# Kernel tuning notes

Hardware: AMD Instinct MI355X
Metric: run time of the kernel (lower is better)

The kernel has to match this reference:

```python
import jax, jax.numpy as jnp
import numpy as np

NEG_SLOPE = 0.2
K_L = 0.5
K_G = 0.5
TEMP_G = 1e-3


def _leaky(v):
    return jnp.where(v >= 0, v, NEG_SLOPE * v)


def _topk_row_mask(scores, keep):
    # scores: [n, n, h]; torch.topk(dim=0) -> indices [keep, n] per head,
    # then head_mask[indices, :] = 1 selects whole ROWS (any column hit).
    n = scores.shape[0]
    s = jnp.transpose(scores, (1, 2, 0))        # [n_cols, h, n_rows]
    _, idx = jax.lax.top_k(s, keep)             # [n_cols, h, keep]

    def per_head(idx_h):                        # idx_h: [n_cols, keep]
        return jnp.zeros((n,), scores.dtype).at[idx_h.reshape(-1)].set(1.0)

    rows = jax.vmap(per_head, in_axes=1, out_axes=0)(idx)  # [h, n_rows]
    return jnp.transpose(rows)[:, None, :]      # [n_rows, 1, h] broadcast over cols


def setup_inputs() -> dict:
    key = jax.random.key(0)
    ks = jax.random.split(key, 8)
    n, in_f, feat_dim = 1024, 256, 128
    H, F = 4, 64                                # n_heads, n_hidden (out_features=256)
    feats = jax.random.normal(ks[0], (n, feat_dim), dtype=jnp.float32)
    x = jax.random.normal(ks[1], (n, in_f), dtype=jnp.float32)
    adj = jax.random.randint(ks[2], (n, n, 1), 0, 2).astype(jnp.int32)
    sc = 0.05
    W_l = jax.random.normal(ks[3], (in_f, H * F), dtype=jnp.float32) * sc
    W_r = jax.random.normal(ks[4], (in_f, H * F), dtype=jnp.float32) * sc
    attn_w = jax.random.normal(ks[5], (F,), dtype=jnp.float32) * sc
    W_delta = jax.random.normal(ks[6], (2 * F, F), dtype=jnp.float32) * sc
    b_delta = jnp.zeros((F,), dtype=jnp.float32)
    return {"feats": feats, "x": x, "adj": adj, "W_l": W_l, "W_r": W_r,
            "attn_w": attn_w, "W_delta": W_delta, "b_delta": b_delta}


def reference(feats, x, adj, W_l, W_r, attn_w, W_delta, b_delta):
    n = x.shape[0]
    F = attn_w.shape[0]
    H = W_l.shape[1] // F
    g_l = (x @ W_l).reshape(n, H, F)
    g_r = (x @ W_r).reshape(n, H, F)
    # g_sum[i, j] = g_l[j] + g_r[i]  (repeat vs repeat_interleave ordering)
    g_sum = g_r[:, None, :, :] + g_l[None, :, :, :]          # [n, n, H, F]
    e = jnp.einsum('ijhf,f->ijh', _leaky(g_sum), attn_w)     # [n, n, H]

    mask_adj = adj > 0                                        # [n, n, 1]
    a_l = jax.nn.softmax(jnp.where(mask_adj, e, -jnp.inf), axis=1)
    a_1nd = a_l * mask_adj.astype(e.dtype)

    keep_l = int(n * (1.0 - K_L))
    a_filt = a_1nd * _topk_row_mask(a_1nd, keep_l)
    attn_local = jnp.einsum('ijh,jhf->ihf', a_filt, g_r)     # [n, H, F]

    omega = jax.nn.softmax(e, axis=1)
    fn = (feats - feats.min(axis=0)) / (feats.max(axis=0) - feats.min(axis=0))
    fn = jnp.where(jnp.isnan(fn), 0.0, fn)
    g_rn = (g_r - g_r.min(axis=0)) / (g_r.max(axis=0) - g_r.min(axis=0))
    nf = jnp.linalg.norm(fn, axis=1)                          # [n] (index j)
    ng = jnp.linalg.norm(g_rn, axis=2)                        # [n, H] (index i)
    alpha = jax.nn.softmax(jnp.abs(nf[None, :, None] - ng[:, None, :]), axis=1)
    gamma = 0.5 * (omega + (1.0 - alpha))

    keep_g = int(n * (1.0 - K_G))
    gf = gamma * _topk_row_mask(gamma, keep_g)
    gf = jax.nn.softmax(jnp.where(gf == 0, 1e-10, gf) / TEMP_G, axis=1)
    attn_global = jnp.einsum('ijh,jhf->ihf', gf, g_r)         # [n, H, F]

    inter = _leaky(jnp.concatenate([attn_local, attn_global], axis=2) @ W_delta + b_delta)
    delta = jax.nn.softmax(inter, axis=1)                     # softmax over heads (torch dim=1)
    attn_res = delta * attn_local + (1.0 - delta) * attn_global
    return attn_res.reshape(n, H * F)
```

## Files before the change

### kernel.cpp

```cpp
#include <hip/hip_runtime.h>
#include <cstdint>
#include <cstddef>

#define N 1024
#define HN 4
#define FDIM 64
#define KSEL 512
#define FLT_MAX_ 3.402823466e+38f

__device__ __forceinline__ float wred_sum(float v){
#pragma unroll
  for(int o=32;o>0;o>>=1) v += __shfl_down(v,o,64);
  return v;
}
__device__ __forceinline__ float bfly_sum(float v){
#pragma unroll
  for(int o=1;o<64;o<<=1) v += __shfl_xor(v,o,64);
  return v;
}
__device__ __forceinline__ float bfly_max(float v){
#pragma unroll
  for(int o=1;o<64;o<<=1) v = fmaxf(v,__shfl_xor(v,o,64));
  return v;
}
__device__ __forceinline__ int bfly_sumi(int v){
#pragma unroll
  for(int o=1;o<64;o<<=1) v += __shfl_xor(v,o,64);
  return v;
}
__device__ __forceinline__ float bred_sum(float v, float* scr){
  int t=threadIdx.x;
  v = wred_sum(v);
  __syncthreads();
  if((t&63)==0) scr[t>>6]=v;
  __syncthreads();
  return (scr[0]+scr[1])+(scr[2]+scr[3]);
}

__global__ __launch_bounds__(256) void stage1(const float* __restrict__ x,
                                              const float* __restrict__ W_l,
                                              const float* __restrict__ W_r,
                                              const int* __restrict__ adj,
                                              const float* __restrict__ feats,
                                              float* __restrict__ g_l,
                                              float* __restrict__ g_r,
                                              unsigned* __restrict__ adjbit,
                                              int* __restrict__ masks,
                                              float* __restrict__ pmin_f,
                                              float* __restrict__ pmax_f){
  int bx = blockIdx.x, t = threadIdx.x;
  if(bx < 512){
    const float* __restrict__ W = (bx >= 256) ? W_r : W_l;
    float* __restrict__ g = (bx >= 256) ? g_r : g_l;
    int i0 = (bx & 255)*4;
    float acc[4] = {0.f,0.f,0.f,0.f};
#pragma unroll 8
    for(int k=0;k<256;k++){
      float w = W[(size_t)k*256 + t];
#pragma unroll
      for(int r=0;r<4;r++) acc[r] = fmaf(x[(size_t)(i0+r)*256 + k], w, acc[r]);
    }
#pragma unroll
    for(int r=0;r<4;r++) g[(size_t)(i0+r)*256 + t] = acc[r];
  } else if(bx < 1536){
    int i = bx - 512, w = t>>6, lane = t&63;
    if(i < 32) masks[i*256 + t] = 0;
#pragma unroll
    for(int it=0; it<4; it++){
      int j = w*256 + it*64 + lane;
      int v = adj[(size_t)i*N + j];
      unsigned long long mb = __ballot(v > 0);
      if(lane == 0){
        adjbit[i*32 + w*8 + it*2]     = (unsigned)mb;
        adjbit[i*32 + w*8 + it*2 + 1] = (unsigned)(mb >> 32);
      }
    }
  } else {
    int chunk = bx - 1536;
    if(t < 128){
      float lo = FLT_MAX_, hi = -FLT_MAX_;
      int r0 = chunk*64;
      for(int r=0;r<64;r++){
        float v = feats[(size_t)(r0+r)*128 + t];
        lo = fminf(lo,v); hi = fmaxf(hi,v);
      }
      pmin_f[chunk*128+t]=lo; pmax_f[chunk*128+t]=hi;
    }
  }
}

__global__ __launch_bounds__(256) void stage2(const float* __restrict__ g_l,
                                              const float* __restrict__ g_r,
                                              const float* __restrict__ attn_w,
                                              const float* __restrict__ feats,
                                              const float* __restrict__ pmin_f, const float* __restrict__ pmax_f,
                                              float* __restrict__ pmin_g, float* __restrict__ pmax_g,
                                              float* __restrict__ nf,
                                              float* __restrict__ e,
                                              float* __restrict__ eT){
  __shared__ __align__(16) float smem[2*64*68 + 128];
  int bx = blockIdx.x, t = threadIdx.x;
  if(bx < 1024){
    float* grs = smem;
    float* gls = smem + 64*68;
    float* aw  = smem + 2*64*68;
    float* aw2 = aw + 64;
    int h = bx >> 8, i0 = ((bx>>4)&15)*64, j0 = (bx&15)*64;
    if(t < 64){ float w = attn_w[t]; aw[t]=w; aw2[t]=0.2f*w; }
#pragma unroll
    for(int k=0;k<16;k++){
      int idx = t + k*256; int r = idx>>6, f = idx&63;
      grs[r*68+f] = g_r[(size_t)(i0+r)*256 + h*64 + f];
      gls[r*68+f] = g_l[(size_t)(j0+r)*256 + h*64 + f];
    }
    __syncthreads();
    int tj = t&15, ti = t>>4;
    float acc[4][4];
#pragma unroll
    for(int a=0;a<4;a++)
#pragma unroll
      for(int b=0;b<4;b++) acc[a][b]=0.f;
    for(int fc=0; fc<64; fc+=4){
      float4 wv  = *(float4*)&aw[fc];
      float4 wv2 = *(float4*)&aw2[fc];
      float4 ga4[4], gb4[4];
#pragma unroll
      for(int a=0;a<4;a++) ga4[a] = *(float4*)&grs[(ti*4+a)*68+fc];
#pragma unroll
      for(int b=0;b<4;b++) gb4[b] = *(float4*)&gls[(tj+16*b)*68+fc];
#pragma unroll
      for(int a=0;a<4;a++)
#pragma unroll
        for(int b=0;b<4;b++){
          float s0 = ga4[a].x + gb4[b].x;
          float s1 = ga4[a].y + gb4[b].y;
          float s2 = ga4[a].z + gb4[b].z;
          float s3 = ga4[a].w + gb4[b].w;
          acc[a][b] = fmaf(s0, (s0>=0.f)?wv.x:wv2.x, acc[a][b]);
          acc[a][b] = fmaf(s1, (s1>=0.f)?wv.y:wv2.y, acc[a][b]);
          acc[a][b] = fmaf(s2, (s2>=0.f)?wv.z:wv2.z, acc[a][b]);
          acc[a][b] = fmaf(s3, (s3>=0.f)?wv.w:wv2.w, acc[a][b]);
        }
    }
#pragma unroll
    for(int a=0;a<4;a++)
#pragma unroll
      for(int b=0;b<4;b++){
        int i = i0 + ti*4 + a, j = j0 + tj + 16*b;
        e[((size_t)h*N + i)*N + j] = acc[a][b];
      }
    __syncthreads();
    float* esT = smem;
#pragma unroll
    for(int a=0;a<4;a++)
#pragma unroll
      for(int b=0;b<4;b++)
        esT[(tj + 16*b)*68 + ti*4 + a] = acc[a][b];
    __syncthreads();
#pragma unroll
    for(int k=0;k<4;k++){
      int jl = (t>>4) + 16*k, ilx = (t&15)*4;
      *(float4*)(eT + ((size_t)h*N + j0 + jl)*N + i0 + ilx) = *(float4*)&esT[jl*68 + ilx];
    }
  } else if(bx < 1040){
    int chunk = bx - 1024;
    float lo = FLT_MAX_, hi = -FLT_MAX_;
    int r0 = chunk*64;
    for(int r=0;r<64;r++){
      float v = g_r[(size_t)(r0+r)*256 + t];
      lo = fminf(lo,v); hi = fmaxf(hi,v);
    }
    pmin_g[chunk*256+t]=lo; pmax_g[chunk*256+t]=hi;
  } else {
    int i = bx - 1040;
    float* scr = smem;
    float u = 0.f;
    if(t < 128){
      float lo = FLT_MAX_, hi = -FLT_MAX_;
#pragma unroll
      for(int k=0;k<16;k++){
        lo = fminf(lo, pmin_f[k*128+t]);
        hi = fmaxf(hi, pmax_f[k*128+t]);
      }
      float d = hi - lo;
      float v = feats[(size_t)i*128 + t];
      u = (d==0.f) ? 0.f : (v - lo)/d;
    }
    float tot = bred_sum(u*u, scr);
    if(t==0) nf[i] = sqrtf(tot);
  }
}

__global__ __launch_bounds__(256) void row_stats(const float* __restrict__ e,
                                                 const unsigned* __restrict__ adjbit,
                                                 const float* __restrict__ nf,
                                                 const float* __restrict__ g_r,
                                                 const float* __restrict__ pmin_g, const float* __restrict__ pmax_g,
                                                 float* __restrict__ ng,
                                                 float* __restrict__ mlA, float* __restrict__ islA,
                                                 float* __restrict__ moA, float* __restrict__ isoA,
                                                 float* __restrict__ maA, float* __restrict__ isaA,
                                                 float* __restrict__ mgA, float* __restrict__ sgA){
  int i = blockIdx.x, t = threadIdx.x, h = t>>6, lane = t&63;
  float glo = FLT_MAX_, ghi = -FLT_MAX_;
#pragma unroll
  for(int k=0;k<16;k++){
    glo = fminf(glo, pmin_g[k*256 + h*64 + lane]);
    ghi = fmaxf(ghi, pmax_g[k*256 + h*64 + lane]);
  }
  float dg = ghi - glo;
  float ug = (g_r[(size_t)i*256 + h*64 + lane] - glo)/dg;
  float ngv = sqrtf(bfly_sum(ug*ug));
  if(lane==0) ng[h*N + i] = ngv;

  size_t base = ((size_t)h*N + i)*N;
  float er[16], nfr[16];
  unsigned nib[4];
#pragma unroll
  for(int c=0;c<4;c++){
    float4 e4 = *(const float4*)(e  + base + c*256 + lane*4);
    float4 n4 = *(const float4*)(nf + c*256 + lane*4);
    er[c*4+0]=e4.x; er[c*4+1]=e4.y; er[c*4+2]=e4.z; er[c*4+3]=e4.w;
    nfr[c*4+0]=n4.x; nfr[c*4+1]=n4.y; nfr[c*4+2]=n4.z; nfr[c*4+3]=n4.w;
    nib[c] = (adjbit[i*32 + c*8 + (lane>>3)] >> ((lane&7)*4)) & 0xFu;
  }
  float ml=-FLT_MAX_, mo=-FLT_MAX_, ma=-FLT_MAX_;
#pragma unroll
  for(int c=0;c<4;c++)
#pragma unroll
    for(int k=0;k<4;k++){
      int q = c*4+k;
      float ev = er[q];
      mo = fmaxf(mo, ev);
      if((nib[c]>>k)&1) ml = fmaxf(ml, ev);
      ma = fmaxf(ma, fabsf(nfr[q]-ngv));
    }
  ml = bfly_max(ml); mo = bfly_max(mo); ma = bfly_max(ma);
  float sl=0.f, so=0.f, sa=0.f;
#pragma unroll
  for(int c=0;c<4;c++)
#pragma unroll
    for(int k=0;k<4;k++){
      int q = c*4+k;
      float ev = er[q];
      so += __expf(ev-mo);
      if((nib[c]>>k)&1) sl += __expf(ev-ml);
      sa += __expf(fabsf(nfr[q]-ngv)-ma);
    }
  sl = bfly_sum(sl); so = bfly_sum(so); sa = bfly_sum(sa);
  float isl = 1.f/sl, iso = 1.f/so, isa = 1.f/sa;
  float gg[16];
  float mg = -FLT_MAX_;
#pragma unroll
  for(int q=0;q<16;q++){
    float ev = er[q];
    float omega = __expf(ev-mo)*iso;
    float alpha = __expf(fabsf(nfr[q]-ngv)-ma)*isa;
    float g = 0.5f*(omega + 1.f - alpha);
    gg[q] = g;
    mg = fmaxf(mg, g);
  }
  mg = bfly_max(mg);
  float sg = 0.f;
#pragma unroll
  for(int q=0;q<16;q++) sg += __expf((gg[q]-mg)/1e-3f);
  sg = bfly_sum(sg);
  if(lane==0){
    mlA[h*N+i]=ml; islA[h*N+i]=isl;
    moA[h*N+i]=mo; isoA[h*N+i]=iso;
    maA[h*N+i]=ma; isaA[h*N+i]=isa;
    mgA[h*N+i]=mg; sgA[h*N+i]=sg;
  }
}

__device__ __forceinline__ void apply_mask(const unsigned* ur, unsigned T, int tneed, int EQ,
                                           int* __restrict__ mask, int base, int lane){
  if(EQ == tneed){
#pragma unroll
    for(int c=0;c<4;c++)
#pragma unroll
      for(int k2=0;k2<4;k2++){
        int i = c*256 + lane*4 + k2;
        if(ur[c*4+k2] >= T) mask[base + i] = 1;
      }
  } else {
    int run_base = 0;
#pragma unroll
    for(int c=0;c<4;c++){
      int tc=0;
      unsigned long long bm[4];
#pragma unroll
      for(int k2=0;k2<4;k2++){
        bm[k2] = __ballot(ur[c*4+k2]==T);
        tc += (ur[c*4+k2]==T)?1:0;
      }
      unsigned long long lower = (lane==0) ? 0ull : (~0ull >> (64-lane));
      int run = run_base;
#pragma unroll
      for(int k2=0;k2<4;k2++) run += (int)__popcll(bm[k2] & lower);
#pragma unroll
      for(int k2=0;k2<4;k2++){
        int i = c*256 + lane*4 + k2;
        unsigned u = ur[c*4+k2];
        bool sel = (u > T) || (u == T && run < tneed);
        run += (u==T)?1:0;
        if(sel) mask[base + i] = 1;
      }
      int ctot = 0;
#pragma unroll
      for(int k2=0;k2<4;k2++) ctot += (int)__popcll(bm[k2]);
      run_base += ctot;
    }
  }
}

__global__ __launch_bounds__(256) void colselect9(const float* __restrict__ eT,
                                                  const unsigned* __restrict__ adjbit,
                                                  const float* __restrict__ nf,
                                                  const float* __restrict__ mlA, const float* __restrict__ islA,
                                                  const float* __restrict__ moA, const float* __restrict__ isoA,
                                                  const float* __restrict__ maA, const float* __restrict__ isaA,
                                                  const float* __restrict__ ngA,
                                                  int* __restrict__ mask_l,
                                                  int* __restrict__ mask_g){
  int t = threadIdx.x, w = t>>6, lane = t&63;
  int gcol = blockIdx.x*4 + w;
  int z  = gcol >> 12;
  int hj = gcol & 4095;
  int h  = hj >> 10, jc = hj & 1023;
  const float* __restrict__ src = eT + (size_t)hj * (size_t)N;

  float ev[16];
#pragma unroll
  for(int c=0;c<4;c++){
    float4 e4 = ((const float4*)src)[c*64 + lane];
    ev[c*4+0]=e4.x; ev[c*4+1]=e4.y; ev[c*4+2]=e4.z; ev[c*4+3]=e4.w;
  }
  unsigned ur[16];
  if(z == 0){
    int wo = jc >> 5; unsigned bm = 1u << (jc & 31);
#pragma unroll
    for(int c=0;c<4;c++){
      int ib = (h<<10) + c*256 + lane*4;
      float4 ml4 = *(const float4*)(mlA+ib);
      float4 il4 = *(const float4*)(islA+ib);
      float mlv[4] = {ml4.x,ml4.y,ml4.z,ml4.w};
      float ilv[4] = {il4.x,il4.y,il4.z,il4.w};
#pragma unroll
      for(int k=0;k<4;k++){
        int i = c*256 + lane*4 + k;
        float a = (adjbit[i*32 + wo] & bm) ? __expf(ev[c*4+k]-mlv[k])*ilv[k] : 0.f;
        ur[c*4+k] = __float_as_uint(a);
      }
    }
  } else {
    float nfv = nf[jc];
#pragma unroll
    for(int c=0;c<4;c++){
      int ib = (h<<10) + c*256 + lane*4;
      float4 mo4 = *(const float4*)(moA+ib);
      float4 io4 = *(const float4*)(isoA+ib);
      float4 ma4 = *(const float4*)(maA+ib);
      float4 ia4 = *(const float4*)(isaA+ib);
      float4 ng4 = *(const float4*)(ngA+ib);
      float mov[4]={mo4.x,mo4.y,mo4.z,mo4.w}, iov[4]={io4.x,io4.y,io4.z,io4.w};
      float mav[4]={ma4.x,ma4.y,ma4.z,ma4.w}, iav[4]={ia4.x,ia4.y,ia4.z,ia4.w};
      float ngv[4]={ng4.x,ng4.y,ng4.z,ng4.w};
#pragma unroll
      for(int k=0;k<4;k++){
        float omega = __expf(ev[c*4+k]-mov[k])*iov[k];
        float alpha = __expf(fabsf(nfv-ngv[k])-mav[k])*iav[k];
        float g = 0.5f*(omega + 1.f - alpha);
        ur[c*4+k] = __float_as_uint(g);
      }
    }
  }

  unsigned prefix = 0u;
  for(int b=30; b>=0; b--){
    unsigned cand = prefix | (1u<<b);
    int c = 0;
#pragma unroll
    for(int q=0;q<16;q++) c += (int)__popcll(__ballot(ur[q] >= cand));
    prefix = (c >= KSEL) ? cand : prefix;
  }
  unsigned T = prefix;
  int GT = 0, EQ = 0;
#pragma unroll
  for(int q=0;q<16;q++){
    GT += (int)__popcll(__ballot(ur[q] > T));
    EQ += (int)__popcll(__ballot(ur[q] == T));
  }
  int tneed = KSEL - GT;

  int* __restrict__ mask = z ? mask_g : mask_l;
  apply_mask(ur, T, tneed, EQ, mask, h<<10, lane);
}

__global__ __launch_bounds__(256) void attn_mm2(const float* __restrict__ eT,
                                                const float* __restrict__ g_r,
                                                const unsigned* __restrict__ adjbit,
                                                const float* __restrict__ nf,
                                                const float* __restrict__ mlA, const float* __restrict__ islA,
                                                const float* __restrict__ moA, const float* __restrict__ isoA,
                                                const float* __restrict__ maA, const float* __restrict__ isaA,
                                                const float* __restrict__ ngA,
                                                const float* __restrict__ mgA, const float* __restrict__ sgA,
                                                const int* __restrict__ mask_g,
                                                float* __restrict__ partL,
                                                float* __restrict__ partG){
  __shared__ __align__(16) float a_t[2][32][36];
  __shared__ __align__(16) float p_t[2][32][36];
  __shared__ __align__(16) float b_s[2][32][68];
  int i0 = blockIdx.x*32, h = blockIdx.y, s = blockIdx.z, j0 = s*128;
  int t = threadIdx.x;
  int il = t & 31, jq = t >> 5;
  int gi = h*N + i0 + il;
  float ml_r = mlA[gi], il_r = islA[gi];
  float mo_r = moA[gi], io_r = isoA[gi];
  float ma_r = maA[gi], ia_r = isaA[gi];
  float ng_r = ngA[gi];
  float mg_r = mgA[gi], isg_r = 1.f/sgA[gi];
  int   mgf_r = mask_g[gi];
  int fq = t & 15, iq = t >> 4;
  int jb2a = t>>4, d4a = t&15;
  int idxb = t + 256, jb2b = idxb>>4, d4b = idxb&15;

  float e0,e1,e2,e3; unsigned aw; float4 nf4, vb0, vb1;
  {
    int jb = j0;
    size_t ebase = ((size_t)h*N + jb + jq*4)*(size_t)N + i0 + il;
    e0 = eT[ebase]; e1 = eT[ebase+N]; e2 = eT[ebase+2*N]; e3 = eT[ebase+3*N];
    aw = adjbit[(size_t)(i0+il)*32 + s*4 + 0];
    nf4 = *(const float4*)(nf + jb + jq*4);
    vb0 = *(const float4*)(g_r + (size_t)(jb+jb2a)*256 + h*64 + d4a*4);
    vb1 = *(const float4*)(g_r + (size_t)(jb+jb2b)*256 + h*64 + d4b*4);
  }
  {
    const float inv = 1.f/1024.f;
    float evs[4] = {e0,e1,e2,e3};
    float nfsv[4] = {nf4.x,nf4.y,nf4.z,nf4.w};
#pragma unroll
    for(int c=0;c<4;c++){
      int jl = jq*4 + c;
      float a = ((aw >> jl) & 1u) ? __expf(evs[c]-ml_r)*il_r : 0.f;
      float omega = __expf(evs[c]-mo_r)*io_r;
      float alpha = __expf(fabsf(nfsv[c]-ng_r)-ma_r)*ia_r;
      float g = 0.5f*(omega + 1.f - alpha);
      float p = mgf_r ? __expf((g-mg_r)/1e-3f)*isg_r : inv;
      a_t[0][jl][il] = a;
      p_t[0][jl][il] = p;
    }
    *(float4*)&b_s[0][jb2a][d4a*4] = vb0;
    *(float4*)&b_s[0][jb2b][d4b*4] = vb1;
  }
  float4 accL[2], accG[2];
#pragma unroll
  for(int r=0;r<2;r++){ accL[r]=make_float4(0,0,0,0); accG[r]=make_float4(0,0,0,0); }

  for(int sub=0; sub<4; sub++){
    int cur = sub & 1;
    __syncthreads();
    if(sub < 3){
      int jb = j0 + (sub+1)*32;
      size_t ebase = ((size_t)h*N + jb + jq*4)*(size_t)N + i0 + il;
      e0 = eT[ebase]; e1 = eT[ebase+N]; e2 = eT[ebase+2*N]; e3 = eT[ebase+3*N];
      aw = adjbit[(size_t)(i0+il)*32 + s*4 + sub + 1];
      nf4 = *(const float4*)(nf + jb + jq*4);
      vb0 = *(const float4*)(g_r + (size_t)(jb+jb2a)*256 + h*64 + d4a*4);
      vb1 = *(const float4*)(g_r + (size_t)(jb+jb2b)*256 + h*64 + d4b*4);
    }
#pragma unroll 8
    for(int j=0;j<32;j++){
      float4 bv = *(float4*)&b_s[cur][j][fq*4];
      float2 av = *(float2*)&a_t[cur][j][iq*2];
      float2 pv = *(float2*)&p_t[cur][j][iq*2];
      accL[0].x = fmaf(av.x, bv.x, accL[0].x); accL[0].y = fmaf(av.x, bv.y, accL[0].y);
      accL[0].z = fmaf(av.x, bv.z, accL[0].z); accL[0].w = fmaf(av.x, bv.w, accL[0].w);
      accL[1].x = fmaf(av.y, bv.x, accL[1].x); accL[1].y = fmaf(av.y, bv.y, accL[1].y);
      accL[1].z = fmaf(av.y, bv.z, accL[1].z); accL[1].w = fmaf(av.y, bv.w, accL[1].w);
      accG[0].x = fmaf(pv.x, bv.x, accG[0].x); accG[0].y = fmaf(pv.x, bv.y, accG[0].y);
      accG[0].z = fmaf(pv.x, bv.z, accG[0].z); accG[0].w = fmaf(pv.x, bv.w, accG[0].w);
      accG[1].x = fmaf(pv.y, bv.x, accG[1].x); accG[1].y = fmaf(pv.y, bv.y, accG[1].y);
      accG[1].z = fmaf(pv.y, bv.z, accG[1].z); accG[1].w = fmaf(pv.y, bv.w, accG[1].w);
    }
    if(sub < 3){
      int nxt = 1 - cur;
      const float inv = 1.f/1024.f;
      float evs[4] = {e0,e1,e2,e3};
      float nfsv[4] = {nf4.x,nf4.y,nf4.z,nf4.w};
#pragma unroll
      for(int c=0;c<4;c++){
        int jl = jq*4 + c;
        float a = ((aw >> jl) & 1u) ? __expf(evs[c]-ml_r)*il_r : 0.f;
        float omega = __expf(evs[c]-mo_r)*io_r;
        float alpha = __expf(fabsf(nfsv[c]-ng_r)-ma_r)*ia_r;
        float g = 0.5f*(omega + 1.f - alpha);
        float p = mgf_r ? __expf((g-mg_r)/1e-3f)*isg_r : inv;
        a_t[nxt][jl][il] = a;
        p_t[nxt][jl][il] = p;
      }
      *(float4*)&b_s[nxt][jb2a][d4a*4] = vb0;
      *(float4*)&b_s[nxt][jb2b][d4b*4] = vb1;
    }
  }
#pragma unroll
  for(int r=0;r<2;r++){
    int i = i0 + iq*2 + r;
    size_t o = ((size_t)s*N + i)*256 + h*64 + fq*4;
    *(float4*)&partL[o] = accL[r];
    *(float4*)&partG[o] = accG[r];
  }
}

__global__ __launch_bounds__(256) void epilogue(const float* __restrict__ partL,
                                                const float* __restrict__ partG,
                                                const int* __restrict__ mask_l,
                                                const float* __restrict__ W_delta,
                                                const float* __restrict__ b_delta,
                                                float* __restrict__ out){
  __shared__ float cat[4][128];
  __shared__ float inter_s[4][64];
  int i = blockIdx.x, t = threadIdx.x;
  int h = t>>6, f = t&63;
  float sl = 0.f, sg = 0.f;
#pragma unroll
  for(int s2=0;s2<8;s2++){
    size_t o = ((size_t)s2*N + i)*256 + h*64 + f;
    sl += partL[o];
    sg += partG[o];
  }
  if(!mask_l[h*N + i]) sl = 0.f;
  cat[h][f]      = sl;
  cat[h][64 + f] = sg;
  __syncthreads();
  float d = b_delta[f];
  for(int c=0;c<128;c++) d = fmaf(cat[h][c], W_delta[(size_t)c*64 + f], d);
  d = (d >= 0.f) ? d : 0.2f*d;
  inter_s[h][f] = d;
  __syncthreads();
  float m = inter_s[0][f];
#pragma unroll
  for(int hh=1;hh<4;hh++) m = fmaxf(m, inter_s[hh][f]);
  float ssum = 0.f;
#pragma unroll
  for(int hh=0;hh<4;hh++) ssum += __expf(inter_s[hh][f]-m);
  float delta = __expf(d - m)/ssum;
  out[(size_t)i*256 + h*64 + f] = delta*sl + (1.f - delta)*sg;
}

extern "C" void kernel_launch(void* const* d_in, const int* in_sizes, int n_in,
                              void* d_out, int out_size, void* d_ws, size_t ws_size,
                              hipStream_t stream) {
  const float* feats  = (const float*)d_in[0];
  const float* x      = (const float*)d_in[1];
  const int*   adj    = (const int*)  d_in[2];
  const float* W_l    = (const float*)d_in[3];
  const float* W_r    = (const float*)d_in[4];
  const float* attn_w = (const float*)d_in[5];
  const float* W_delta= (const float*)d_in[6];
  const float* b_delta= (const float*)d_in[7];
  float* out = (float*)d_out;

  float* ws = (float*)d_ws;
  size_t off = 0;
  float* g_l   = ws+off; off += (size_t)N*256;
  float* g_r   = ws+off; off += (size_t)N*256;
  float* e     = ws+off; off += (size_t)HN*N*N;
  float* eT    = ws+off; off += (size_t)HN*N*N;
  float* partL = ws+off; off += (size_t)8*N*256;
  float* partG = ws+off; off += (size_t)8*N*256;
  float* pmin_f= ws+off; off += 16*128;
  float* pmax_f= ws+off; off += 16*128;
  float* pmin_g= ws+off; off += 16*256;
  float* pmax_g= ws+off; off += 16*256;
  float* nf    = ws+off; off += N;
  float* ng    = ws+off; off += (size_t)HN*N;
  float* mlA   = ws+off; off += (size_t)HN*N;
  float* islA  = ws+off; off += (size_t)HN*N;
  float* moA   = ws+off; off += (size_t)HN*N;
  float* isoA  = ws+off; off += (size_t)HN*N;
  float* maA   = ws+off; off += (size_t)HN*N;
  float* isaA  = ws+off; off += (size_t)HN*N;
  float* mgA   = ws+off; off += (size_t)HN*N;
  float* sgA   = ws+off; off += (size_t)HN*N;
  int* mask_l  = (int*)(ws+off); off += (size_t)HN*N;
  int* mask_g  = (int*)(ws+off); off += (size_t)HN*N;
  unsigned* adjbit = (unsigned*)(ws+off); off += (size_t)N*32;

  stage1<<<1552, 256, 0, stream>>>(x, W_l, W_r, adj, feats, g_l, g_r, adjbit, mask_l, pmin_f, pmax_f);

  stage2<<<2064, 256, 0, stream>>>(g_l, g_r, attn_w, feats, pmin_f, pmax_f,
                                   pmin_g, pmax_g, nf, e, eT);

  row_stats<<<N, 256, 0, stream>>>(e, adjbit, nf, g_r, pmin_g, pmax_g, ng,
                                   mlA, islA, moA, isoA, maA, isaA, mgA, sgA);

  colselect9<<<2048, 256, 0, stream>>>(eT, adjbit, nf, mlA, islA, moA, isoA,
                                       maA, isaA, ng, mask_l, mask_g);

  attn_mm2<<<dim3(32,HN,8), 256, 0, stream>>>(eT, g_r, adjbit, nf,
                                              mlA, islA, moA, isoA, maA, isaA, ng,
                                              mgA, sgA, mask_g, partL, partG);

  epilogue<<<N, 256, 0, stream>>>(partL, partG, mask_l, W_delta, b_delta, out);
}
```

Measured before the change: 193.9 us.

## Merge top-k column selection into attention matmul kernel, defer global mask to epilogue

Removes the dependency of the attention matmul on the global top-k mask. The matmul now always computes the temperature-softmax weights, and the epilogue replaces unmasked rows with the column mean of g_r, built from per-chunk sums added to stage2. The selection work and the matmul then run as independent blocks of one launch, so they overlap and one kernel launch disappears. The trade-offs are extra exp work on masked-out rows and a larger, mixed grid.

```diff
diff --git a/kernel.cpp b/kernel.cpp
--- a/kernel.cpp
+++ b/kernel.cpp
@@ -21,11 +21,6 @@
 __device__ __forceinline__ float bfly_max(float v){
 #pragma unroll
   for(int o=1;o<64;o<<=1) v = fmaxf(v,__shfl_xor(v,o,64));
-  return v;
-}
-__device__ __forceinline__ int bfly_sumi(int v){
-#pragma unroll
-  for(int o=1;o<64;o<<=1) v += __shfl_xor(v,o,64);
   return v;
 }
 __device__ __forceinline__ float bred_sum(float v, float* scr){
@@ -95,6 +90,7 @@
                                               const float* __restrict__ feats,
                                               const float* __restrict__ pmin_f, const float* __restrict__ pmax_f,
                                               float* __restrict__ pmin_g, float* __restrict__ pmax_g,
+                                              float* __restrict__ psum_g,
                                               float* __restrict__ nf,
                                               float* __restrict__ e,
                                               float* __restrict__ eT){
@@ -164,13 +160,13 @@
     }
   } else if(bx < 1040){
     int chunk = bx - 1024;
-    float lo = FLT_MAX_, hi = -FLT_MAX_;
+    float lo = FLT_MAX_, hi = -FLT_MAX_, sm = 0.f;
     int r0 = chunk*64;
     for(int r=0;r<64;r++){
       float v = g_r[(size_t)(r0+r)*256 + t];
-      lo = fminf(lo,v); hi = fmaxf(hi,v);
-    }
-    pmin_g[chunk*256+t]=lo; pmax_g[chunk*256+t]=hi;
+      lo = fminf(lo,v); hi = fmaxf(hi,v); sm += v;
+    }
+    pmin_g[chunk*256+t]=lo; pmax_g[chunk*256+t]=hi; psum_g[chunk*256+t]=sm;
   } else {
     int i = bx - 1040;
     float* scr = smem;
@@ -287,13 +283,9 @@
     int run_base = 0;
 #pragma unroll
     for(int c=0;c<4;c++){
-      int tc=0;
       unsigned long long bm[4];
 #pragma unroll
-      for(int k2=0;k2<4;k2++){
-        bm[k2] = __ballot(ur[c*4+k2]==T);
-        tc += (ur[c*4+k2]==T)?1:0;
-      }
+      for(int k2=0;k2<4;k2++) bm[k2] = __ballot(ur[c*4+k2]==T);
       unsigned long long lower = (lane==0) ? 0ull : (~0ull >> (64-lane));
       int run = run_base;
 #pragma unroll
@@ -314,106 +306,103 @@
   }
 }
 
-__global__ __launch_bounds__(256) void colselect9(const float* __restrict__ eT,
-                                                  const unsigned* __restrict__ adjbit,
-                                                  const float* __restrict__ nf,
-                                                  const float* __restrict__ mlA, const float* __restrict__ islA,
-                                                  const float* __restrict__ moA, const float* __restrict__ isoA,
-                                                  const float* __restrict__ maA, const float* __restrict__ isaA,
-                                                  const float* __restrict__ ngA,
-                                                  int* __restrict__ mask_l,
-                                                  int* __restrict__ mask_g){
-  int t = threadIdx.x, w = t>>6, lane = t&63;
-  int gcol = blockIdx.x*4 + w;
-  int z  = gcol >> 12;
-  int hj = gcol & 4095;
-  int h  = hj >> 10, jc = hj & 1023;
-  const float* __restrict__ src = eT + (size_t)hj * (size_t)N;
-
-  float ev[16];
-#pragma unroll
-  for(int c=0;c<4;c++){
-    float4 e4 = ((const float4*)src)[c*64 + lane];
-    ev[c*4+0]=e4.x; ev[c*4+1]=e4.y; ev[c*4+2]=e4.z; ev[c*4+3]=e4.w;
-  }
-  unsigned ur[16];
-  if(z == 0){
-    int wo = jc >> 5; unsigned bm = 1u << (jc & 31);
-#pragma unroll
-    for(int c=0;c<4;c++){
-      int ib = (h<<10) + c*256 + lane*4;
-      float4 ml4 = *(const float4*)(mlA+ib);
-      float4 il4 = *(const float4*)(islA+ib);
-      float mlv[4] = {ml4.x,ml4.y,ml4.z,ml4.w};
-      float ilv[4] = {il4.x,il4.y,il4.z,il4.w};
-#pragma unroll
-      for(int k=0;k<4;k++){
-        int i = c*256 + lane*4 + k;
-        float a = (adjbit[i*32 + wo] & bm) ? __expf(ev[c*4+k]-mlv[k])*ilv[k] : 0.f;
-        ur[c*4+k] = __float_as_uint(a);
-      }
-    }
-  } else {
-    float nfv = nf[jc];
-#pragma unroll
-    for(int c=0;c<4;c++){
-      int ib = (h<<10) + c*256 + lane*4;
-      float4 mo4 = *(const float4*)(moA+ib);
-      float4 io4 = *(const float4*)(isoA+ib);
-      float4 ma4 = *(const float4*)(maA+ib);
-      float4 ia4 = *(const float4*)(isaA+ib);
-      float4 ng4 = *(const float4*)(ngA+ib);
-      float mov[4]={mo4.x,mo4.y,mo4.z,mo4.w}, iov[4]={io4.x,io4.y,io4.z,io4.w};
-      float mav[4]={ma4.x,ma4.y,ma4.z,ma4.w}, iav[4]={ia4.x,ia4.y,ia4.z,ia4.w};
-      float ngv[4]={ng4.x,ng4.y,ng4.z,ng4.w};
-#pragma unroll
-      for(int k=0;k<4;k++){
-        float omega = __expf(ev[c*4+k]-mov[k])*iov[k];
-        float alpha = __expf(fabsf(nfv-ngv[k])-mav[k])*iav[k];
-        float g = 0.5f*(omega + 1.f - alpha);
-        ur[c*4+k] = __float_as_uint(g);
-      }
-    }
-  }
-
-  unsigned prefix = 0u;
-  for(int b=30; b>=0; b--){
-    unsigned cand = prefix | (1u<<b);
-    int c = 0;
-#pragma unroll
-    for(int q=0;q<16;q++) c += (int)__popcll(__ballot(ur[q] >= cand));
-    prefix = (c >= KSEL) ? cand : prefix;
-  }
-  unsigned T = prefix;
-  int GT = 0, EQ = 0;
-#pragma unroll
-  for(int q=0;q<16;q++){
-    GT += (int)__popcll(__ballot(ur[q] > T));
-    EQ += (int)__popcll(__ballot(ur[q] == T));
-  }
-  int tneed = KSEL - GT;
-
-  int* __restrict__ mask = z ? mask_g : mask_l;
-  apply_mask(ur, T, tneed, EQ, mask, h<<10, lane);
-}
-
-__global__ __launch_bounds__(256) void attn_mm2(const float* __restrict__ eT,
-                                                const float* __restrict__ g_r,
-                                                const unsigned* __restrict__ adjbit,
-                                                const float* __restrict__ nf,
-                                                const float* __restrict__ mlA, const float* __restrict__ islA,
-                                                const float* __restrict__ moA, const float* __restrict__ isoA,
-                                                const float* __restrict__ maA, const float* __restrict__ isaA,
-                                                const float* __restrict__ ngA,
-                                                const float* __restrict__ mgA, const float* __restrict__ sgA,
-                                                const int* __restrict__ mask_g,
-                                                float* __restrict__ partL,
-                                                float* __restrict__ partG){
+__global__ __launch_bounds__(256) void mm_sel(const float* __restrict__ eT,
+                                              const float* __restrict__ g_r,
+                                              const unsigned* __restrict__ adjbit,
+                                              const float* __restrict__ nf,
+                                              const float* __restrict__ mlA, const float* __restrict__ islA,
+                                              const float* __restrict__ moA, const float* __restrict__ isoA,
+                                              const float* __restrict__ maA, const float* __restrict__ isaA,
+                                              const float* __restrict__ ngA,
+                                              const float* __restrict__ mgA, const float* __restrict__ sgA,
+                                              float* __restrict__ partL,
+                                              float* __restrict__ partG,
+                                              int* __restrict__ mask_l,
+                                              int* __restrict__ mask_g){
   __shared__ __align__(16) float a_t[2][32][36];
   __shared__ __align__(16) float p_t[2][32][36];
   __shared__ __align__(16) float b_s[2][32][68];
-  int i0 = blockIdx.x*32, h = blockIdx.y, s = blockIdx.z, j0 = s*128;
+  int bx = blockIdx.x, h = blockIdx.y, s = blockIdx.z;
   int t = threadIdx.x;
+
+  if(bx >= 32){
+    int w = t>>6, lane = t&63;
+    int sid = (bx - 32) + 64*(h + 4*s);
+    int gcol = sid*4 + w;
+    int z  = gcol >> 12;
+    int hj = gcol & 4095;
+    int hh = hj >> 10, jc = hj & 1023;
+    const float* __restrict__ src = eT + (size_t)hj * (size_t)N;
+
+    float ev[16];
+#pragma unroll
+    for(int c=0;c<4;c++){
+      float4 e4 = ((const float4*)src)[c*64 + lane];
+      ev[c*4+0]=e4.x; ev[c*4+1]=e4.y; ev[c*4+2]=e4.z; ev[c*4+3]=e4.w;
+    }
+    unsigned ur[16];
+    if(z == 0){
+      int wo = jc >> 5; unsigned bm = 1u << (jc & 31);
+#pragma unroll
+      for(int c=0;c<4;c++){
+        int ib = (hh<<10) + c*256 + lane*4;
+        float4 ml4 = *(const float4*)(mlA+ib);
+        float4 il4 = *(const float4*)(islA+ib);
+        float mlv[4] = {ml4.x,ml4.y,ml4.z,ml4.w};
+        float ilv[4] = {il4.x,il4.y,il4.z,il4.w};
+#pragma unroll
+        for(int k=0;k<4;k++){
+          int i = c*256 + lane*4 + k;
+          float a = (adjbit[i*32 + wo] & bm) ? __expf(ev[c*4+k]-mlv[k])*ilv[k] : 0.f;
+          ur[c*4+k] = __float_as_uint(a);
+        }
+      }
+    } else {
+      float nfv = nf[jc];
+#pragma unroll
+      for(int c=0;c<4;c++){
+        int ib = (hh<<10) + c*256 + lane*4;
+        float4 mo4 = *(const float4*)(moA+ib);
+        float4 io4 = *(const float4*)(isoA+ib);
+        float4 ma4 = *(const float4*)(maA+ib);
+        float4 ia4 = *(const float4*)(isaA+ib);
+        float4 ng4 = *(const float4*)(ngA+ib);
+        float mov[4]={mo4.x,mo4.y,mo4.z,mo4.w}, iov[4]={io4.x,io4.y,io4.z,io4.w};
+        float mav[4]={ma4.x,ma4.y,ma4.z,ma4.w}, iav[4]={ia4.x,ia4.y,ia4.z,ia4.w};
+        float ngv[4]={ng4.x,ng4.y,ng4.z,ng4.w};
+#pragma unroll
+        for(int k=0;k<4;k++){
+          float omega = __expf(ev[c*4+k]-mov[k])*iov[k];
+          float alpha = __expf(fabsf(nfv-ngv[k])-mav[k])*iav[k];
+          float g = 0.5f*(omega + 1.f - alpha);
+          ur[c*4+k] = __float_as_uint(g);
+        }
+      }
+    }
+
+    unsigned prefix = 0u;
+    for(int b=30; b>=0; b--){
+      unsigned cand = prefix | (1u<<b);
+      int c = 0;
+#pragma unroll
+      for(int q=0;q<16;q++) c += (int)__popcll(__ballot(ur[q] >= cand));
+      prefix = (c >= KSEL) ? cand : prefix;
+    }
+    unsigned T = prefix;
+    int GT = 0, EQ = 0;
+#pragma unroll
+    for(int q=0;q<16;q++){
+      GT += (int)__popcll(__ballot(ur[q] > T));
+      EQ += (int)__popcll(__ballot(ur[q] == T));
+    }
+    int tneed = KSEL - GT;
+
+    int* __restrict__ mask = z ? mask_g : mask_l;
+    apply_mask(ur, T, tneed, EQ, mask, hh<<10, lane);
+    return;
+  }
+
+  int i0 = bx*32, j0 = s*128;
   int il = t & 31, jq = t >> 5;
   int gi = h*N + i0 + il;
   float ml_r = mlA[gi], il_r = islA[gi];
@@ -421,7 +410,6 @@
   float ma_r = maA[gi], ia_r = isaA[gi];
   float ng_r = ngA[gi];
   float mg_r = mgA[gi], isg_r = 1.f/sgA[gi];
-  int   mgf_r = mask_g[gi];
   int fq = t & 15, iq = t >> 4;
   int jb2a = t>>4, d4a = t&15;
   int idxb = t + 256, jb2b = idxb>>4, d4b = idxb&15;
@@ -437,7 +425,6 @@
     vb1 = *(const float4*)(g_r + (size_t)(jb+jb2b)*256 + h*64 + d4b*4);
   }
   {
-    const float inv = 1.f/1024.f;
     float evs[4] = {e0,e1,e2,e3};
     float nfsv[4] = {nf4.x,nf4.y,nf4.z,nf4.w};
 #pragma unroll
@@ -447,7 +434,7 @@
       float omega = __expf(evs[c]-mo_r)*io_r;
       float alpha = __expf(fabsf(nfsv[c]-ng_r)-ma_r)*ia_r;
       float g = 0.5f*(omega + 1.f - alpha);
-      float p = mgf_r ? __expf((g-mg_r)/1e-3f)*isg_r : inv;
+      float p = __expf((g-mg_r)/1e-3f)*isg_r;
       a_t[0][jl][il] = a;
       p_t[0][jl][il] = p;
     }
@@ -486,7 +473,6 @@
     }
     if(sub < 3){
       int nxt = 1 - cur;
-      const float inv = 1.f/1024.f;
       float evs[4] = {e0,e1,e2,e3};
       float nfsv[4] = {nf4.x,nf4.y,nf4.z,nf4.w};
 #pragma unroll
@@ -496,7 +482,7 @@
         float omega = __expf(evs[c]-mo_r)*io_r;
         float alpha = __expf(fabsf(nfsv[c]-ng_r)-ma_r)*ia_r;
         float g = 0.5f*(omega + 1.f - alpha);
-        float p = mgf_r ? __expf((g-mg_r)/1e-3f)*isg_r : inv;
+        float p = __expf((g-mg_r)/1e-3f)*isg_r;
         a_t[nxt][jl][il] = a;
         p_t[nxt][jl][il] = p;
       }
@@ -516,6 +502,8 @@
 __global__ __launch_bounds__(256) void epilogue(const float* __restrict__ partL,
                                                 const float* __restrict__ partG,
                                                 const int* __restrict__ mask_l,
+                                                const int* __restrict__ mask_g,
+                                                const float* __restrict__ psum_g,
                                                 const float* __restrict__ W_delta,
                                                 const float* __restrict__ b_delta,
                                                 float* __restrict__ out){
@@ -531,6 +519,12 @@
     sg += partG[o];
   }
   if(!mask_l[h*N + i]) sl = 0.f;
+  if(!mask_g[h*N + i]){
+    float gs = 0.f;
+#pragma unroll
+    for(int k=0;k<16;k++) gs += psum_g[k*256 + t];
+    sg = gs * (1.f/1024.f);
+  }
   cat[h][f]      = sl;
   cat[h][64 + f] = sg;
   __syncthreads();
@@ -574,6 +568,7 @@
   float* pmax_f= ws+off; off += 16*128;
   float* pmin_g= ws+off; off += 16*256;
   float* pmax_g= ws+off; off += 16*256;
+  float* psum_g= ws+off; off += 16*256;
   float* nf    = ws+off; off += N;
   float* ng    = ws+off; off += (size_t)HN*N;
   float* mlA   = ws+off; off += (size_t)HN*N;
@@ -591,17 +586,14 @@
   stage1<<<1552, 256, 0, stream>>>(x, W_l, W_r, adj, feats, g_l, g_r, adjbit, mask_l, pmin_f, pmax_f);
 
   stage2<<<2064, 256, 0, stream>>>(g_l, g_r, attn_w, feats, pmin_f, pmax_f,
-                                   pmin_g, pmax_g, nf, e, eT);
+                                   pmin_g, pmax_g, psum_g, nf, e, eT);
 
   row_stats<<<N, 256, 0, stream>>>(e, adjbit, nf, g_r, pmin_g, pmax_g, ng,
                                    mlA, islA, moA, isoA, maA, isaA, mgA, sgA);
 
-  colselect9<<<2048, 256, 0, stream>>>(eT, adjbit, nf, mlA, islA, moA, isoA,
-                                       maA, isaA, ng, mask_l, mask_g);
-
-  attn_mm2<<<dim3(32,HN,8), 256, 0, stream>>>(eT, g_r, adjbit, nf,
-                                              mlA, islA, moA, isoA, maA, isaA, ng,
-                                              mgA, sgA, mask_g, partL, partG);
-
-  epilogue<<<N, 256, 0, stream>>>(partL, partG, mask_l, W_delta, b_delta, out);
-}
+  mm_sel<<<dim3(96,HN,8), 256, 0, stream>>>(eT, g_r, adjbit, nf,
+                                            mlA, islA, moA, isoA, maA, isaA, ng,
+                                            mgA, sgA, partL, partG, mask_l, mask_g);
+
+  epilogue<<<N, 256, 0, stream>>>(partL, partG, mask_l, mask_g, psum_g, W_delta, b_delta, out);
+}
```

Result: faster. 181.2 us (median of 2 runs) (-6.6%).
